# Kernel tuning notes

Measured on AMD Instinct MI355X. Metric: run time of the kernel, lower is better.

Reference implementation:

```python
import jax, jax.numpy as jnp
import numpy as np

PATCH = 8
GROUPS = 32
EPS = 1e-5


def group_norm(x, gamma, beta):
    # x: [B, C, H, W]; GroupNorm over (C//G, H, W) per group per sample
    B, C, H, W = x.shape
    xr = x.reshape(B, GROUPS, C // GROUPS, H, W)
    mu = xr.mean(axis=(2, 3, 4), keepdims=True)
    var = xr.var(axis=(2, 3, 4), keepdims=True)
    xn = ((xr - mu) * jax.lax.rsqrt(var + EPS)).reshape(B, C, H, W)
    return xn * gamma[None, :, None, None] + beta[None, :, None, None]


def patchify(x, p):
    # [B, C, H, W] -> [(B h w), C, p*p]  (matches einops 'b c (h p1) (w p2) -> (b h w) c (p1 p2)')
    B, C, H, W = x.shape
    h, w = H // p, W // p
    return x.reshape(B, C, h, p, w, p).transpose(0, 2, 4, 1, 3, 5).reshape(B * h * w, C, p * p)


def setup_inputs() -> dict:
    key = jax.random.key(0)
    ks = jax.random.split(key, 4)
    B, C, H, W = 8, 256, 128, 128
    x_low = jax.random.normal(ks[0], (B, C, H, W), dtype=jnp.float32)
    x_high = jax.random.normal(ks[1], (B, C, H, W), dtype=jnp.float32)
    # 1x1 conv weights [out_c, in_c] (kernel size 1 squeezed), no bias
    Wq = jax.random.normal(ks[2], (C, C), dtype=jnp.float32) / np.sqrt(C)
    Wk = jax.random.normal(ks[3], (C, C), dtype=jnp.float32) / np.sqrt(C)
    gq = jnp.ones((C,), jnp.float32)
    bq = jnp.zeros((C,), jnp.float32)
    gk = jnp.ones((C,), jnp.float32)
    bk = jnp.zeros((C,), jnp.float32)
    return {"x_low": x_low, "x_high": x_high, "Wq": Wq, "gq": gq, "bq": bq,
            "Wk": Wk, "gk": gk, "bk": bk}


def reference(x_low, x_high, Wq, gq, bq, Wk, gk, bk):
    p = PATCH
    B, C, H, W = x_low.shape
    h, w = H // p, W // p
    # conv_q / conv_k: 1x1 conv (no bias) + GroupNorm(32)
    qf = group_norm(jnp.einsum('bchw,oc->bohw', x_low, Wq), gq, bq)
    kf = group_norm(jnp.einsum('bchw,oc->bohw', x_high, Wk), gk, bk)
    q = patchify(qf, p).transpose(0, 2, 1)   # [N, P2, C]
    k = patchify(kf, p)                      # [N, C, P2]
    scale = jnp.asarray(np.power(C, 0.5), jnp.float32)
    attn = jax.nn.softmax(jnp.einsum('npc,ncq->npq', q, k) / scale, axis=-1)  # [N, P2, P2]
    out = jnp.einsum('npq,nqc->npc', attn, k.transpose(0, 2, 1))  # [N, P2, C], v = k^T
    # '(b h w) c (p1 p2) -> b c (h p1) (w p2)'
    out = out.reshape(B, h, w, p, p, C).transpose(0, 5, 1, 3, 2, 4).reshape(B, C, H, W)
    return out + x_low
```

## Files before the change

### kernel.cpp

```cpp
#include <hip/hip_runtime.h>
#include <cstdint>
#include <cstddef>

#define B_N   8
#define C_N   256
#define H_N   128
#define W_N   128
#define S_N   16384
#define CS_N  4194304
#define NELEM 33554432
#define EPS_F 1e-5f

typedef __attribute__((ext_vector_type(8))) short short8;
typedef __attribute__((ext_vector_type(4))) float f32x4;

union PackB { uint32_t w[4]; uint4 u4; short8 s8; };

__device__ __forceinline__ uint32_t bf16_rne(float x) {
  const uint32_t u = __float_as_uint(x);
  return (u + 0x7FFFu + ((u >> 16) & 1u)) >> 16;
}
__device__ __forceinline__ uint32_t splitpack(float x) {
  const uint32_t hi = bf16_rne(x);
  const float r = x - __uint_as_float(hi << 16);
  const uint32_t lo = bf16_rne(r);
  return (hi << 16) | lo;
}
__device__ __forceinline__ int swz(int s, int c) {
  return (s * 64 + c) ^ (((s & 3) << 3) | (s & 4));
}

__global__ __launch_bounds__(256) void prep_w(
    const float* __restrict__ Wq, const float* __restrict__ Wk,
    uint4* __restrict__ wpk)
{
  const int gid = blockIdx.x * 256 + threadIdx.x;
  const int lane = gid & 63;
  const int f = gid >> 6;
  const int hl = f & 1;
  const int mf = (f >> 1) & 15;
  const int kf = (f >> 5) & 7;
  const int tensor = (f >> 8) & 1;
  const float* __restrict__ Wsrc = tensor ? Wk : Wq;

  const int o  = mf * 16 + (lane & 15);
  const int c0 = kf * 32 + ((lane >> 4) << 3);
  const float* src = Wsrc + (size_t)o * 256 + c0;
  const float4 x0 = *reinterpret_cast<const float4*>(src);
  const float4 x1 = *reinterpret_cast<const float4*>(src + 4);
  const float xs[8] = {x0.x, x0.y, x0.z, x0.w, x1.x, x1.y, x1.z, x1.w};

  uint32_t h[8];
#pragma unroll
  for (int e = 0; e < 8; ++e) {
    const uint32_t hi = bf16_rne(xs[e]);
    if (hl == 0) {
      h[e] = hi;
    } else {
      h[e] = bf16_rne(xs[e] - __uint_as_float(hi << 16));
    }
  }
  uint4 outw;
  outw.x = h[0] | (h[1] << 16);
  outw.y = h[2] | (h[3] << 16);
  outw.z = h[4] | (h[5] << 16);
  outw.w = h[6] | (h[7] << 16);
  wpk[(size_t)f * 64 + lane] = outw;
}

__global__ __launch_bounds__(256) void conv_mfma(
    const float* __restrict__ x_low, const float* __restrict__ x_high,
    const uint4* __restrict__ wpk,
    float* __restrict__ qf, float* __restrict__ kf)
{
  const int t = threadIdx.x;
  const int lane = t & 63;
  const int w = t >> 6;
  const int tile = blockIdx.x;
  const int bz = blockIdx.y;
  const int tensor = bz >> 3;
  const int b = bz & 7;

  const float* __restrict__ X = tensor ? x_high : x_low;
  float* __restrict__ Y = tensor ? kf : qf;
  const short8* __restrict__ wpkS = reinterpret_cast<const short8*>(wpk);

  const size_t xbase = (size_t)b * CS_N;
  const int s0 = tile * 64;

  __shared__ uint32_t xb[2][4096];

  const int cl = t >> 2;
  const int sq = t & 3;
  int offA, offB;
  if (tensor) {
    const int rA = 2 * sq, rB = 2 * sq + 1;
    const int pb = ((tile >> 4) << 3) * W_N + ((tile & 15) << 3);
    offA = pb + rA * W_N;
    offB = pb + rB * W_N;
  } else {
    offA = s0 + sq * 16;
    offB = offA + 8;
  }
  const float* __restrict__ Xb = X + xbase;

  f32x4 acc[4][4] = {};

  auto stage_write = [&](const float4& A0, const float4& A1,
                         const float4& B0, const float4& B1, int nb) {
    const float v[16] = {A0.x, A0.y, A0.z, A0.w, A1.x, A1.y, A1.z, A1.w,
                         B0.x, B0.y, B0.z, B0.w, B1.x, B1.y, B1.z, B1.w};
#pragma unroll
    for (int jj = 0; jj < 16; ++jj) {
      const int sl = sq * 16 + jj;
      xb[nb][swz(sl, cl)] = splitpack(v[jj]);
    }
  };

  {
    const float* p = Xb + (size_t)cl * S_N;
    const float4 A0 = *reinterpret_cast<const float4*>(p + offA);
    const float4 A1 = *reinterpret_cast<const float4*>(p + offA + 4);
    const float4 B0 = *reinterpret_cast<const float4*>(p + offB);
    const float4 B1 = *reinterpret_cast<const float4*>(p + offB + 4);
    stage_write(A0, A1, B0, B1, 0);
  }

  for (int kt = 0; kt < 4; ++kt) {
    const int cur = kt & 1;
    __syncthreads();

    float4 nA0, nA1, nB0, nB1;
    if (kt < 3) {
      const float* p = Xb + (size_t)((kt + 1) * 64 + cl) * S_N;
      nA0 = *reinterpret_cast<const float4*>(p + offA);
      nA1 = *reinterpret_cast<const float4*>(p + offA + 4);
      nB0 = *reinterpret_cast<const float4*>(p + offB);
      nB1 = *reinterpret_cast<const float4*>(p + offB + 4);
    }

#pragma unroll
    for (int ks = 0; ks < 2; ++ks) {
      const int kfrag = kt * 2 + ks;
      const int fbase = ((tensor * 8 + kfrag) * 16 + w * 4) * 2;
      short8 a_hi[4], a_lo[4];
#pragma unroll
      for (int mf = 0; mf < 4; ++mf) {
        a_hi[mf] = wpkS[(size_t)(fbase + mf * 2) * 64 + lane];
        a_lo[mf] = wpkS[(size_t)(fbase + mf * 2 + 1) * 64 + lane];
      }
      short8 b_hi[4], b_lo[4];
      const int c0 = ks * 32 + ((lane >> 4) << 3);
#pragma unroll
      for (int nf = 0; nf < 4; ++nf) {
        const int sl = nf * 16 + (lane & 15);
        const int wx = ((sl & 3) << 3) | (sl & 4);
        const int base1 = ((sl * 64 + c0) ^ wx);
        const int base2 = ((sl * 64 + c0 + 4) ^ wx);
        const uint4 u = *reinterpret_cast<const uint4*>(&xb[cur][base1]);
        const uint4 v = *reinterpret_cast<const uint4*>(&xb[cur][base2]);
        PackB ph, pl;
        ph.w[0] = __builtin_amdgcn_perm(u.y, u.x, 0x07060302u);
        ph.w[1] = __builtin_amdgcn_perm(u.w, u.z, 0x07060302u);
        ph.w[2] = __builtin_amdgcn_perm(v.y, v.x, 0x07060302u);
        ph.w[3] = __builtin_amdgcn_perm(v.w, v.z, 0x07060302u);
        pl.w[0] = __builtin_amdgcn_perm(u.y, u.x, 0x05040100u);
        pl.w[1] = __builtin_amdgcn_perm(u.w, u.z, 0x05040100u);
        pl.w[2] = __builtin_amdgcn_perm(v.y, v.x, 0x05040100u);
        pl.w[3] = __builtin_amdgcn_perm(v.w, v.z, 0x05040100u);
        b_hi[nf] = ph.s8;
        b_lo[nf] = pl.s8;
      }
#pragma unroll
      for (int mf = 0; mf < 4; ++mf)
#pragma unroll
        for (int nf = 0; nf < 4; ++nf) {
          acc[mf][nf] = __builtin_amdgcn_mfma_f32_16x16x32_bf16(
              a_hi[mf], b_hi[nf], acc[mf][nf], 0, 0, 0);
          acc[mf][nf] = __builtin_amdgcn_mfma_f32_16x16x32_bf16(
              a_hi[mf], b_lo[nf], acc[mf][nf], 0, 0, 0);
          acc[mf][nf] = __builtin_amdgcn_mfma_f32_16x16x32_bf16(
              a_lo[mf], b_hi[nf], acc[mf][nf], 0, 0, 0);
        }
    }

    if (kt < 3) stage_write(nA0, nA1, nB0, nB1, cur ^ 1);
  }

  const int orow = w * 64 + ((lane >> 4) << 2);
  const int scol = s0 + (lane & 15);
#pragma unroll
  for (int mf = 0; mf < 4; ++mf)
#pragma unroll
    for (int nf = 0; nf < 4; ++nf) {
      const int o = orow + mf * 16;
      const int s = scol + nf * 16;
#pragma unroll
      for (int r = 0; r < 4; ++r)
        Y[xbase + (size_t)(o + r) * S_N + s] = acc[mf][nf][r];
    }
}

__global__ __launch_bounds__(256) void gn_stats(
    const float* __restrict__ qf, const float* __restrict__ kf,
    float2* __restrict__ stats)
{
  const int bid = blockIdx.x;
  const int tensor = bid >> 8;
  const int rem = bid & 255;
  const int b = rem >> 5;
  const int g = rem & 31;
  const float* __restrict__ base =
      (tensor ? kf : qf) + (size_t)b * CS_N + (size_t)g * 8 * S_N;
  const float4* __restrict__ base4 = reinterpret_cast<const float4*>(base);

  const int tid = threadIdx.x;
  float s1 = 0.0f, s2 = 0.0f;
  for (int i = tid; i < 32768; i += 256) {
    const float4 u = base4[i];
    s1 += u.x + u.y + u.z + u.w;
    s2 += u.x * u.x + u.y * u.y + u.z * u.z + u.w * u.w;
  }
#pragma unroll
  for (int off = 32; off > 0; off >>= 1) {
    s1 += __shfl_down(s1, off);
    s2 += __shfl_down(s2, off);
  }
  __shared__ float r1[4], r2[4];
  const int wave = tid >> 6;
  if ((tid & 63) == 0) { r1[wave] = s1; r2[wave] = s2; }
  __syncthreads();
  if (tid == 0) {
    const float S1 = r1[0] + r1[1] + r1[2] + r1[3];
    const float S2 = r2[0] + r2[1] + r2[2] + r2[3];
    const float mean = S1 * (1.0f / 131072.0f);
    const float var = S2 * (1.0f / 131072.0f) - mean * mean;
    stats[bid] = make_float2(mean, rsqrtf(var + EPS_F));
  }
}

__global__ __launch_bounds__(256) void attn_kernel(
    const float* __restrict__ x_low,
    const float* __restrict__ gq, const float* __restrict__ bq,
    const float* __restrict__ gk, const float* __restrict__ bk,
    const float* __restrict__ qf, const float* __restrict__ kf,
    const float2* __restrict__ stats, float* __restrict__ out)
{
  const int n = ((blockIdx.x & 7) << 8) | (blockIdx.x >> 3);
  const int b = n >> 8;
  const int nl = n & 255;
  const int h0 = (nl >> 4) << 3, w0 = (nl & 15) << 3;
  const int t = threadIdx.x;
  const int tx = t & 15, ty = t >> 4;
  const int p = t & 63;
  const int ci = t >> 6;

  __shared__ float q_ch[64][68];
  __shared__ float k_ch[64][68];
  __shared__ float s_mat[64][68];
  __shared__ float red[4][64];
  __shared__ float rowstat[2][64];

  const int lc = t >> 2;
  const int lp = (t & 3) << 4;

  const size_t kbase = (size_t)b * CS_N + ((size_t)nl << 6) + lp;
  const size_t pixoff =
      (size_t)b * CS_N + (size_t)(h0 + (p >> 3)) * W_N + (w0 + (p & 7));

  float accs[4][4];
#pragma unroll
  for (int i = 0; i < 4; ++i)
#pragma unroll
    for (int j = 0; j < 4; ++j) accs[i][j] = 0.0f;

  for (int chunk = 0; chunk < 4; ++chunk) {
    __syncthreads();
    {
      const int c = (chunk << 6) + lc;
      const float2 sk = stats[256 + (b << 5) + (c >> 3)];
      const float ksc = gk[c] * sk.y;
      const float ksh = bk[c] - sk.x * ksc;
      const float4* src = reinterpret_cast<const float4*>(kf + kbase + (size_t)c * S_N);
      const float4 v0 = src[0], v1 = src[1], v2 = src[2], v3 = src[3];
      float4* dst = reinterpret_cast<float4*>(&k_ch[lc][lp]);
      dst[0] = make_float4(fmaf(v0.x, ksc, ksh), fmaf(v0.y, ksc, ksh),
                           fmaf(v0.z, ksc, ksh), fmaf(v0.w, ksc, ksh));
      dst[1] = make_float4(fmaf(v1.x, ksc, ksh), fmaf(v1.y, ksc, ksh),
                           fmaf(v1.z, ksc, ksh), fmaf(v1.w, ksc, ksh));
      dst[2] = make_float4(fmaf(v2.x, ksc, ksh), fmaf(v2.y, ksc, ksh),
                           fmaf(v2.z, ksc, ksh), fmaf(v2.w, ksc, ksh));
      dst[3] = make_float4(fmaf(v3.x, ksc, ksh), fmaf(v3.y, ksc, ksh),
                           fmaf(v3.z, ksc, ksh), fmaf(v3.w, ksc, ksh));
    }
    for (int cl = ci; cl < 64; cl += 4) {
      const int c = (chunk << 6) + cl;
      const float2 sq = stats[(b << 5) + (c >> 3)];
      const float qsc = gq[c] * sq.y * 0.0625f;
      const float qsh = (bq[c] - sq.x * gq[c] * sq.y) * 0.0625f;
      q_ch[cl][p] = fmaf(qf[pixoff + (size_t)c * S_N], qsc, qsh);
    }
    __syncthreads();
#pragma unroll 4
    for (int c = 0; c < 64; ++c) {
      const float4 qv = *reinterpret_cast<const float4*>(&q_ch[c][ty * 4]);
      const float4 kv = *reinterpret_cast<const float4*>(&k_ch[c][tx * 4]);
      const float qa[4] = {qv.x, qv.y, qv.z, qv.w};
      const float ka[4] = {kv.x, kv.y, kv.z, kv.w};
#pragma unroll
      for (int i = 0; i < 4; ++i)
#pragma unroll
        for (int j = 0; j < 4; ++j) accs[i][j] = fmaf(qa[i], ka[j], accs[i][j]);
    }
  }
#pragma unroll
  for (int j = 0; j < 4; ++j)
    *reinterpret_cast<float4*>(&s_mat[tx * 4 + j][ty * 4]) =
        make_float4(accs[0][j], accs[1][j], accs[2][j], accs[3][j]);
  __syncthreads();

  {
    float m = -3.0e38f;
#pragma unroll
    for (int rr = 0; rr < 16; ++rr) m = fmaxf(m, s_mat[ci * 16 + rr][p]);
    red[ci][p] = m;
    __syncthreads();
    if (t < 64)
      rowstat[0][t] = fmaxf(fmaxf(red[0][t], red[1][t]), fmaxf(red[2][t], red[3][t]));
    __syncthreads();
    const float rm = rowstat[0][p];
    float sum = 0.0f;
#pragma unroll
    for (int rr = 0; rr < 16; ++rr) {
      const float e = __expf(s_mat[ci * 16 + rr][p] - rm);
      s_mat[ci * 16 + rr][p] = e;
      sum += e;
    }
    red[ci][p] = sum;
    __syncthreads();
    if (t < 64) rowstat[1][t] = red[0][t] + red[1][t] + red[2][t] + red[3][t];
    __syncthreads();
  }
  const float rinv = 1.0f / rowstat[1][p];

  for (int chunk = 0; chunk < 4; ++chunk) {
    __syncthreads();
    {
      const int c = (chunk << 6) + lc;
      const float2 sk = stats[256 + (b << 5) + (c >> 3)];
      const float ksc = gk[c] * sk.y;
      const float ksh = bk[c] - sk.x * ksc;
      const float4* src = reinterpret_cast<const float4*>(kf + kbase + (size_t)c * S_N);
      const float4 v0 = src[0], v1 = src[1], v2 = src[2], v3 = src[3];
      const float vals[16] = {v0.x, v0.y, v0.z, v0.w, v1.x, v1.y, v1.z, v1.w,
                              v2.x, v2.y, v2.z, v2.w, v3.x, v3.y, v3.z, v3.w};
#pragma unroll
      for (int u = 0; u < 16; ++u) k_ch[lp + u][lc] = fmaf(vals[u], ksc, ksh);
    }
    __syncthreads();
    float accp[4][4];
#pragma unroll
    for (int i = 0; i < 4; ++i)
#pragma unroll
      for (int j = 0; j < 4; ++j) accp[i][j] = 0.0f;
#pragma unroll 4
    for (int r = 0; r < 64; ++r) {
      const float4 pv = *reinterpret_cast<const float4*>(&s_mat[r][ty * 4]);
      const float4 kv = *reinterpret_cast<const float4*>(&k_ch[r][tx * 4]);
      const float pa[4] = {pv.x, pv.y, pv.z, pv.w};
      const float ka[4] = {kv.x, kv.y, kv.z, kv.w};
#pragma unroll
      for (int i = 0; i < 4; ++i)
#pragma unroll
        for (int j = 0; j < 4; ++j) accp[i][j] = fmaf(pa[i], ka[j], accp[i][j]);
    }
#pragma unroll
    for (int i = 0; i < 4; ++i)
      *reinterpret_cast<float4*>(&q_ch[ty * 4 + i][tx * 4]) =
          make_float4(accp[i][0], accp[i][1], accp[i][2], accp[i][3]);
    __syncthreads();
    for (int cl = ci; cl < 64; cl += 4) {
      const size_t a = pixoff + (size_t)((chunk << 6) + cl) * S_N;
      out[a] = fmaf(q_ch[p][cl], rinv, x_low[a]);
    }
  }
}

extern "C" void kernel_launch(void* const* d_in, const int* in_sizes, int n_in,
                              void* d_out, int out_size, void* d_ws, size_t ws_size,
                              hipStream_t stream)
{
  const float* x_low  = (const float*)d_in[0];
  const float* x_high = (const float*)d_in[1];
  const float* Wq     = (const float*)d_in[2];
  const float* gq     = (const float*)d_in[3];
  const float* bq     = (const float*)d_in[4];
  const float* Wk     = (const float*)d_in[5];
  const float* gk     = (const float*)d_in[6];
  const float* bk     = (const float*)d_in[7];
  float* out = (float*)d_out;

  float* qf = out;
  float* kf = (float*)d_ws;
  float2* stats = (float2*)((char*)d_ws + (size_t)NELEM * 4);
  uint4* wpk = (uint4*)((char*)d_ws + (size_t)NELEM * 4 + 4096);

  hipLaunchKernelGGL(prep_w, dim3(128), dim3(256), 0, stream, Wq, Wk, wpk);
  hipLaunchKernelGGL(conv_mfma, dim3(256, 16), dim3(256), 0, stream,
                     x_low, x_high, wpk, qf, kf);
  hipLaunchKernelGGL(gn_stats, dim3(512), dim3(256), 0, stream, qf, kf, stats);
  hipLaunchKernelGGL(attn_kernel, dim3(2048), dim3(256), 0, stream,
                     x_low, gq, bq, gk, bk, qf, kf, stats, out);
}
```

Baseline: 694.2 us.

## Fuse GroupNorm statistics into conv epilogue via atomics, drop stats kernel

The separate gn_stats pass, which re-read both 128 MB conv outputs, is removed. Each conv block now reduces per-group sums and sums of squares from its MFMA accumulators with wave shuffles and atomically adds them into a zeroed stats buffer. The attention kernel derives mean and rsqrt variance from those sums. The change also adds a new LDS swizzle, a remapped staging thread layout and a remapped tile order, in exchange for atomic contention, a memset launch and a less stable E[x^2]-mean^2 computation in float.

New measurement: 771.0 us. 11.1% more time.

```diff
diff --git a/kernel.cpp b/kernel.cpp
--- a/kernel.cpp
+++ b/kernel.cpp
@@ -27,7 +27,7 @@
   return (hi << 16) | lo;
 }
 __device__ __forceinline__ int swz(int s, int c) {
-  return (s * 64 + c) ^ (((s & 3) << 3) | (s & 4));
+  return (s * 64 + c) ^ ((((s & 7) ^ ((s >> 4) & 3)) << 2));
 }
 
 __global__ __launch_bounds__(256) void prep_w(
@@ -71,12 +71,13 @@
 __global__ __launch_bounds__(256) void conv_mfma(
     const float* __restrict__ x_low, const float* __restrict__ x_high,
     const uint4* __restrict__ wpk,
-    float* __restrict__ qf, float* __restrict__ kf)
+    float* __restrict__ qf, float* __restrict__ kf,
+    float2* __restrict__ stats)
 {
   const int t = threadIdx.x;
   const int lane = t & 63;
   const int w = t >> 6;
-  const int tile = blockIdx.x;
+  const int tile = ((blockIdx.x & 7) << 5) | (blockIdx.x >> 3);
   const int bz = blockIdx.y;
   const int tensor = bz >> 3;
   const int b = bz & 7;
@@ -90,8 +91,8 @@
 
   __shared__ uint32_t xb[2][4096];
 
-  const int cl = t >> 2;
-  const int sq = t & 3;
+  const int cl = lane;
+  const int sq = w;
   int offA, offB;
   if (tensor) {
     const int rA = 2 * sq, rB = 2 * sq + 1;
@@ -154,9 +155,8 @@
 #pragma unroll
       for (int nf = 0; nf < 4; ++nf) {
         const int sl = nf * 16 + (lane & 15);
-        const int wx = ((sl & 3) << 3) | (sl & 4);
-        const int base1 = ((sl * 64 + c0) ^ wx);
-        const int base2 = ((sl * 64 + c0 + 4) ^ wx);
+        const int base1 = swz(sl, c0);
+        const int base2 = swz(sl, c0 + 4);
         const uint4 u = *reinterpret_cast<const uint4*>(&xb[cur][base1]);
         const uint4 v = *reinterpret_cast<const uint4*>(&xb[cur][base2]);
         PackB ph, pl;
@@ -199,43 +199,38 @@
       for (int r = 0; r < 4; ++r)
         Y[xbase + (size_t)(o + r) * S_N + s] = acc[mf][nf][r];
     }
-}
-
-__global__ __launch_bounds__(256) void gn_stats(
-    const float* __restrict__ qf, const float* __restrict__ kf,
-    float2* __restrict__ stats)
-{
-  const int bid = blockIdx.x;
-  const int tensor = bid >> 8;
-  const int rem = bid & 255;
-  const int b = rem >> 5;
-  const int g = rem & 31;
-  const float* __restrict__ base =
-      (tensor ? kf : qf) + (size_t)b * CS_N + (size_t)g * 8 * S_N;
-  const float4* __restrict__ base4 = reinterpret_cast<const float4*>(base);
-
-  const int tid = threadIdx.x;
-  float s1 = 0.0f, s2 = 0.0f;
-  for (int i = tid; i < 32768; i += 256) {
-    const float4 u = base4[i];
-    s1 += u.x + u.y + u.z + u.w;
-    s2 += u.x * u.x + u.y * u.y + u.z * u.z + u.w * u.w;
-  }
-#pragma unroll
-  for (int off = 32; off > 0; off >>= 1) {
-    s1 += __shfl_down(s1, off);
-    s2 += __shfl_down(s2, off);
-  }
-  __shared__ float r1[4], r2[4];
-  const int wave = tid >> 6;
-  if ((tid & 63) == 0) { r1[wave] = s1; r2[wave] = s2; }
-  __syncthreads();
-  if (tid == 0) {
-    const float S1 = r1[0] + r1[1] + r1[2] + r1[3];
-    const float S2 = r2[0] + r2[1] + r2[2] + r2[3];
-    const float mean = S1 * (1.0f / 131072.0f);
-    const float var = S2 * (1.0f / 131072.0f) - mean * mean;
-    stats[bid] = make_float2(mean, rsqrtf(var + EPS_F));
+
+  float s1g[4], s2g[4];
+#pragma unroll
+  for (int mf = 0; mf < 4; ++mf) {
+    float a = 0.0f, q = 0.0f;
+#pragma unroll
+    for (int nf = 0; nf < 4; ++nf)
+#pragma unroll
+      for (int r = 0; r < 4; ++r) {
+        const float v = acc[mf][nf][r];
+        a += v;
+        q = fmaf(v, v, q);
+      }
+    s1g[mf] = a; s2g[mf] = q;
+  }
+#pragma unroll
+  for (int off = 16; off >= 1; off >>= 1) {
+#pragma unroll
+    for (int mf = 0; mf < 4; ++mf) {
+      s1g[mf] += __shfl_xor(s1g[mf], off);
+      s2g[mf] += __shfl_xor(s2g[mf], off);
+    }
+  }
+  if ((lane & 31) == 0) {
+    const int hi = lane >> 5;
+    float2* st = stats + (tensor * 256 + b * 32);
+#pragma unroll
+    for (int mf = 0; mf < 4; ++mf) {
+      const int g = w * 8 + mf * 2 + hi;
+      atomicAdd(&st[g].x, s1g[mf]);
+      atomicAdd(&st[g].y, s2g[mf]);
+    }
   }
 }
 
@@ -268,6 +263,8 @@
   const size_t pixoff =
       (size_t)b * CS_N + (size_t)(h0 + (p >> 3)) * W_N + (w0 + (p & 7));
 
+  const float inv_n = 1.0f / 131072.0f;
+
   float accs[4][4];
 #pragma unroll
   for (int i = 0; i < 4; ++i)
@@ -279,8 +276,10 @@
     {
       const int c = (chunk << 6) + lc;
       const float2 sk = stats[256 + (b << 5) + (c >> 3)];
-      const float ksc = gk[c] * sk.y;
-      const float ksh = bk[c] - sk.x * ksc;
+      const float mk = sk.x * inv_n;
+      const float rk = rsqrtf(fmaf(-mk, mk, sk.y * inv_n) + EPS_F);
+      const float ksc = gk[c] * rk;
+      const float ksh = bk[c] - mk * ksc;
       const float4* src = reinterpret_cast<const float4*>(kf + kbase + (size_t)c * S_N);
       const float4 v0 = src[0], v1 = src[1], v2 = src[2], v3 = src[3];
       float4* dst = reinterpret_cast<float4*>(&k_ch[lc][lp]);
@@ -296,8 +295,10 @@
     for (int cl = ci; cl < 64; cl += 4) {
       const int c = (chunk << 6) + cl;
       const float2 sq = stats[(b << 5) + (c >> 3)];
-      const float qsc = gq[c] * sq.y * 0.0625f;
-      const float qsh = (bq[c] - sq.x * gq[c] * sq.y) * 0.0625f;
+      const float mq = sq.x * inv_n;
+      const float rq = rsqrtf(fmaf(-mq, mq, sq.y * inv_n) + EPS_F);
+      const float qsc = gq[c] * rq * 0.0625f;
+      const float qsh = (bq[c] - mq * gq[c] * rq) * 0.0625f;
       q_ch[cl][p] = fmaf(qf[pixoff + (size_t)c * S_N], qsc, qsh);
     }
     __syncthreads();
@@ -348,8 +349,10 @@
     {
       const int c = (chunk << 6) + lc;
       const float2 sk = stats[256 + (b << 5) + (c >> 3)];
-      const float ksc = gk[c] * sk.y;
-      const float ksh = bk[c] - sk.x * ksc;
+      const float mk = sk.x * inv_n;
+      const float rk = rsqrtf(fmaf(-mk, mk, sk.y * inv_n) + EPS_F);
+      const float ksc = gk[c] * rk;
+      const float ksh = bk[c] - mk * ksc;
       const float4* src = reinterpret_cast<const float4*>(kf + kbase + (size_t)c * S_N);
       const float4 v0 = src[0], v1 = src[1], v2 = src[2], v3 = src[3];
       const float vals[16] = {v0.x, v0.y, v0.z, v0.w, v1.x, v1.y, v1.z, v1.w,
@@ -405,10 +408,10 @@
   float2* stats = (float2*)((char*)d_ws + (size_t)NELEM * 4);
   uint4* wpk = (uint4*)((char*)d_ws + (size_t)NELEM * 4 + 4096);
 
+  hipMemsetAsync(stats, 0, 512 * sizeof(float2), stream);
   hipLaunchKernelGGL(prep_w, dim3(128), dim3(256), 0, stream, Wq, Wk, wpk);
   hipLaunchKernelGGL(conv_mfma, dim3(256, 16), dim3(256), 0, stream,
-                     x_low, x_high, wpk, qf, kf);
-  hipLaunchKernelGGL(gn_stats, dim3(512), dim3(256), 0, stream, qf, kf, stats);
+                     x_low, x_high, wpk, qf, kf, stats);
   hipLaunchKernelGGL(attn_kernel, dim3(2048), dim3(256), 0, stream,
                      x_low, gq, bq, gk, bk, qf, kf, stats, out);
 }
```
